# Performance work log

Measured on AMD Instinct MI355X. Metric: run time of the kernel, lower is better.

Reference implementation:

```python
import jax, jax.numpy as jnp
import numpy as np

N = 100000      # nodes
E = 1600000     # edges
D_IN = 16       # input_dim
D_H = 32        # hidden_dim
D_OUT = 1       # output_dim
N_ITERS = 2
D_CAT = D_H + D_IN          # node feature after cat([H, X])
D_EDGE = 2 * D_CAT          # edge MLP input dim


def setup_inputs() -> dict:
    key = jax.random.key(0)
    ks = jax.random.split(key, 10)
    x = jax.random.normal(ks[0], (N, D_IN), jnp.float32)
    edge_index = jax.random.randint(ks[1], (2, E), 0, N, dtype=jnp.int32)
    # inputnet: Linear(D_IN -> D_H) + Tanh
    W_in = jax.random.normal(ks[2], (D_H, D_IN), jnp.float32) / np.sqrt(D_IN)
    b_in = jnp.zeros((D_H,), jnp.float32)
    # convnn (EdgeConv nn): Linear(D_EDGE -> D_H) + Sigmoid
    W_c = jax.random.normal(ks[3], (D_H, D_EDGE), jnp.float32) / np.sqrt(D_EDGE)
    b_c = jnp.zeros((D_H,), jnp.float32)
    # outputnet: Linear(D_H -> D_OUT) + Sigmoid
    W_out = jax.random.normal(ks[4], (D_OUT, D_H), jnp.float32) / np.sqrt(D_H)
    b_out = jnp.zeros((D_OUT,), jnp.float32)
    return {"x": x, "edge_index": edge_index, "W_in": W_in, "b_in": b_in,
            "W_c": W_c, "b_c": b_c, "W_out": W_out, "b_out": b_out}


def reference(x, edge_index, W_in, b_in, W_c, b_c, W_out, b_out):
    src = edge_index[0]  # x_j (source / neighbor)
    dst = edge_index[1]  # x_i (target, aggregation index)

    H = jnp.tanh(x @ W_in.T + b_in)            # [N, D_H]
    feats = jnp.concatenate([H, x], axis=-1)    # [N, D_CAT]

    for _ in range(N_ITERS):
        xi = feats[dst]                          # [E, D_CAT] gather targets
        xj = feats[src]                          # [E, D_CAT] gather sources
        # PyG EdgeConv message: nn(cat([x_i, x_j - x_i]))
        msg = jax.nn.sigmoid(
            jnp.concatenate([xi, xj - xi], axis=-1) @ W_c.T + b_c)  # [E, D_H]
        H = jax.ops.segment_sum(msg, dst, num_segments=N)           # aggr='add'
        feats = jnp.concatenate([H, x], axis=-1)

    sum_H = jnp.mean(H, axis=0)                  # [D_H]
    return jax.nn.sigmoid(sum_H @ W_out.T + b_out)  # [D_OUT]
```

## Files before the change

kernel.cpp:

```cpp
#include <hip/hip_runtime.h>
#include <hip/hip_fp16.h>

#define D_H 32
#define NREP 32
#define SLOTS 48
#define BIN_SHIFT 8
#define MAXNB 512
#define BIN_CAP 5120
#define SB 256
#define PNPB 64
#define SF 52
#define L2E 1.4426950408889634f


__global__ __launch_bounds__(256) void k_ab0(const float* __restrict__ x,
                      const float* __restrict__ W_in, const float* __restrict__ b_in,
                      const float* __restrict__ W_c, const float* __restrict__ b_c,
                      float* __restrict__ A, __half* __restrict__ Bh, int N) {
    __shared__ float f[PNPB][SF];
    int tid = threadIdx.x;
    int n0 = blockIdx.x * PNPB;
    int wv = tid >> 6;
    int h  = (tid >> 5) & 1;
    int j  = tid & 31;
    float wc[96];
    {
        const float4* wr = (const float4*)(W_c + j * 96);
#pragma unroll
        for (int q = 0; q < 24; ++q) {
            float4 v = wr[q];
            wc[4 * q] = v.x; wc[4 * q + 1] = v.y; wc[4 * q + 2] = v.z; wc[4 * q + 3] = v.w;
        }
    }
    float win[16];
    {
        const float4* wr = (const float4*)(W_in + j * 16);
#pragma unroll
        for (int q = 0; q < 4; ++q) {
            float4 v = wr[q];
            win[4 * q] = v.x; win[4 * q + 1] = v.y; win[4 * q + 2] = v.z; win[4 * q + 3] = v.w;
        }
    }
    float bc = b_c[j];
    float bi = b_in[j];
    {
        int row = tid >> 2, c = tid & 3;
        float4 v = {0.f, 0.f, 0.f, 0.f};
        if (n0 + row < N) v = ((const float4*)(x + (size_t)(n0 + row) * 16))[c];
        *(float4*)&f[row][32 + 4 * c] = v;
    }
    __syncthreads();
#pragma unroll 2
    for (int it = 0; it < 8; ++it) {
        int n = wv * 16 + it * 2 + h;
        {
            float4 x0 = *(const float4*)&f[n][32];
            float4 x1 = *(const float4*)&f[n][36];
            float4 x2 = *(const float4*)&f[n][40];
            float4 x3 = *(const float4*)&f[n][44];
            float acc = bi;
            acc += x0.x * win[0] + x0.y * win[1] + x0.z * win[2] + x0.w * win[3];
            acc += x1.x * win[4] + x1.y * win[5] + x1.z * win[6] + x1.w * win[7];
            acc += x2.x * win[8] + x2.y * win[9] + x2.z * win[10] + x2.w * win[11];
            acc += x3.x * win[12] + x3.y * win[13] + x3.z * win[14] + x3.w * win[15];
            f[n][j] = tanhf(acc);
        }
        float p = bc, bb = 0.f;
#pragma unroll
        for (int q = 0; q < 12; ++q) {
            float4 v = *(const float4*)&f[n][4 * q];
            p  += v.x * wc[4 * q]      + v.y * wc[4 * q + 1]
                + v.z * wc[4 * q + 2]  + v.w * wc[4 * q + 3];
            bb += v.x * wc[48 + 4 * q]     + v.y * wc[48 + 4 * q + 1]
                + v.z * wc[48 + 4 * q + 2] + v.w * wc[48 + 4 * q + 3];
        }
        int g = n0 + n;
        if (g < N) {
            A[(size_t)g * D_H + j]  = -L2E * (p - bb);
            Bh[(size_t)g * D_H + j] = __float2half_rn(-L2E * bb);
        }
    }
}

__global__ __launch_bounds__(256) void k_ab1(const float* __restrict__ H,
                      const float* __restrict__ x, const float* __restrict__ W_c,
                      const float* __restrict__ b_c, float* __restrict__ A,
                      __half* __restrict__ Bh, int N) {
    __shared__ float f[PNPB][SF];
    int tid = threadIdx.x;
    int n0 = blockIdx.x * PNPB;
    int wv = tid >> 6;
    int h  = (tid >> 5) & 1;
    int j  = tid & 31;
    float wc[96];
    {
        const float4* wr = (const float4*)(W_c + j * 96);
#pragma unroll
        for (int q = 0; q < 24; ++q) {
            float4 v = wr[q];
            wc[4 * q] = v.x; wc[4 * q + 1] = v.y; wc[4 * q + 2] = v.z; wc[4 * q + 3] = v.w;
        }
    }
    float bc = b_c[j];
#pragma unroll
    for (int k = 0; k < 2; ++k) {
        int i = k * 256 + tid;
        int row = i >> 3, c = i & 7;
        float4 v = {0.f, 0.f, 0.f, 0.f};
        if (n0 + row < N) v = ((const float4*)(H + (size_t)(n0 + row) * D_H))[c];
        *(float4*)&f[row][4 * c] = v;
    }
    {
        int row = tid >> 2, c = tid & 3;
        float4 v = {0.f, 0.f, 0.f, 0.f};
        if (n0 + row < N) v = ((const float4*)(x + (size_t)(n0 + row) * 16))[c];
        *(float4*)&f[row][32 + 4 * c] = v;
    }
    __syncthreads();
#pragma unroll 2
    for (int it = 0; it < 8; ++it) {
        int n = wv * 16 + it * 2 + h;
        float p = bc, bb = 0.f;
#pragma unroll
        for (int q = 0; q < 12; ++q) {
            float4 v = *(const float4*)&f[n][4 * q];
            p  += v.x * wc[4 * q]      + v.y * wc[4 * q + 1]
                + v.z * wc[4 * q + 2]  + v.w * wc[4 * q + 3];
            bb += v.x * wc[48 + 4 * q]     + v.y * wc[48 + 4 * q + 1]
                + v.z * wc[48 + 4 * q + 2] + v.w * wc[48 + 4 * q + 3];
        }
        int g = n0 + n;
        if (g < N) {
            A[(size_t)g * D_H + j]  = -L2E * (p - bb);
            Bh[(size_t)g * D_H + j] = __float2half_rn(-L2E * bb);
        }
    }
}

__global__ __launch_bounds__(256) void k_bin(const int* __restrict__ src,
                                             const int* __restrict__ dst,
                                             int* __restrict__ binCnt,
                                             unsigned int* __restrict__ ebuf, int E) {
    __shared__ int hist[MAXNB];
    int tid = threadIdx.x;
    for (int i = tid; i < MAXNB; i += 256) hist[i] = 0;
    __syncthreads();
    int chunk = (E + SB - 1) / SB;
    int lo = blockIdx.x * chunk;
    int hi = lo + chunk; if (hi > E) hi = E;
    for (int e = lo + tid; e < hi; e += 256) {
        int b = dst[e] >> BIN_SHIFT;
        atomicAdd(&hist[b], 1);
    }
    __syncthreads();
    for (int b = tid; b < MAXNB; b += 256) {
        int c = hist[b];
        int base = c ? atomicAdd(&binCnt[b], c) : 0;
        hist[b] = b * BIN_CAP + base;
    }
    __syncthreads();
    for (int e = lo + tid; e < hi; e += 256) {
        int d = dst[e];
        int s = src[e];
        int b = d >> BIN_SHIFT;
        int pos = atomicAdd(&hist[b], 1);
        if ((unsigned)(pos - b * BIN_CAP) < (unsigned)BIN_CAP)
            ebuf[pos] = ((unsigned)(d & 255) << 24) | (unsigned)s;
    }
}

__global__ __launch_bounds__(256) void k_place(const int* __restrict__ binCnt,
                                               const unsigned int* __restrict__ ebuf,
                                               int* __restrict__ ssrcp,
                                               int* __restrict__ cntG,
                                               float* __restrict__ Srep, int N) {
    __shared__ int cnt[256];
    int tid = threadIdx.x;
    int w = blockIdx.x;
    if (w == 0) {
        float4 z = {0.f, 0.f, 0.f, 0.f};
        ((float4*)Srep)[tid] = z;
    }
    cnt[tid] = 0;
    __syncthreads();
    int n = binCnt[w]; if (n > BIN_CAP) n = BIN_CAP;
    int base = w * BIN_CAP;
    for (int j = tid; j < n; j += 256) {
        unsigned int v = ebuf[base + j];
        int ld = v >> 24;
        int s = v & 0xFFFFFF;
        int slot = atomicAdd(&cnt[ld], 1);
        if (slot < SLOTS)
            ssrcp[(size_t)((w << BIN_SHIFT) + ld) * SLOTS + slot] = s;
    }
    __syncthreads();
    int node = (w << BIN_SHIFT) + tid;
    if (node < N) {
        int c = cnt[tid] < SLOTS ? cnt[tid] : SLOTS;
        cntG[node] = c;
        int cp = (c + 3) & ~3;
        for (int t2 = c; t2 < cp; ++t2)
            ssrcp[(size_t)node * SLOTS + t2] = 0;
    }
}


__global__ __launch_bounds__(256) void k_gather1(const int* __restrict__ cntG,
                          const int* __restrict__ ssrcp,
                          const float* __restrict__ A, const __half* __restrict__ Bh,
                          float* __restrict__ H, int N) {
    int t = blockIdx.x * blockDim.x + threadIdx.x;
    int d = t >> 5;
    if (d >= N) return;
    int l = t & 31;
    int q = l & 7;
    int s = l >> 3;
    int len = cntG[d];
    const int* base = ssrcp + (size_t)d * SLOTS;
    float4 a4 = ((const float4*)(A + (size_t)d * D_H))[q];
    float4 acc = {0.f, 0.f, 0.f, 0.f};
    for (int bj = 0; bj < len; bj += 16) {
        int jj = bj + 4 * s;
        if (jj < len) {
            int4 iv = *(const int4*)(base + jj);
            int rem = len - jj;
#pragma unroll
            for (int k = 0; k < 4; ++k) {
                int idx = ((const int*)&iv)[k];
                float vld = (k < rem) ? 1.f : 0.f;
                uint2 u = *(const uint2*)(Bh + (size_t)idx * D_H + 4 * q);
                __half2 h0 = *reinterpret_cast<const __half2*>(&u.x);
                __half2 h1 = *reinterpret_cast<const __half2*>(&u.y);
                float2 f0 = __half22float2(h0);
                float2 f1 = __half22float2(h1);
                float e0 = exp2f(a4.x + f0.x);
                float e1 = exp2f(a4.y + f0.y);
                float e2 = exp2f(a4.z + f1.x);
                float e3 = exp2f(a4.w + f1.y);
                acc.x = fmaf(vld, __builtin_amdgcn_rcpf(1.f + e0), acc.x);
                acc.y = fmaf(vld, __builtin_amdgcn_rcpf(1.f + e1), acc.y);
                acc.z = fmaf(vld, __builtin_amdgcn_rcpf(1.f + e2), acc.z);
                acc.w = fmaf(vld, __builtin_amdgcn_rcpf(1.f + e3), acc.w);
            }
        }
    }
    acc.x += __shfl_xor(acc.x, 8);  acc.y += __shfl_xor(acc.y, 8);
    acc.z += __shfl_xor(acc.z, 8);  acc.w += __shfl_xor(acc.w, 8);
    acc.x += __shfl_xor(acc.x, 16); acc.y += __shfl_xor(acc.y, 16);
    acc.z += __shfl_xor(acc.z, 16); acc.w += __shfl_xor(acc.w, 16);
    if (s == 0) ((float4*)(H + (size_t)d * D_H))[q] = acc;
}

__global__ __launch_bounds__(256) void k_gather2(const int* __restrict__ cntG,
                          const int* __restrict__ ssrcp,
                          const float* __restrict__ A, const __half* __restrict__ Bh,
                          float* __restrict__ Srep, int N) {
    int l = threadIdx.x & 31;
    int slot = threadIdx.x >> 5;
    int q = l & 7;
    int s = l >> 3;
    int d = blockIdx.x * 8 + slot;
    float4 acc = {0.f, 0.f, 0.f, 0.f};
    if (d < N) {
        int len = cntG[d];
        const int* base = ssrcp + (size_t)d * SLOTS;
        float4 a4 = ((const float4*)(A + (size_t)d * D_H))[q];
        for (int bj = 0; bj < len; bj += 16) {
            int jj = bj + 4 * s;
            if (jj < len) {
                int4 iv = *(const int4*)(base + jj);
                int rem = len - jj;
#pragma unroll
                for (int k = 0; k < 4; ++k) {
                    int idx = ((const int*)&iv)[k];
                    float vld = (k < rem) ? 1.f : 0.f;
                    uint2 u = *(const uint2*)(Bh + (size_t)idx * D_H + 4 * q);
                    __half2 h0 = *reinterpret_cast<const __half2*>(&u.x);
                    __half2 h1 = *reinterpret_cast<const __half2*>(&u.y);
                    float2 f0 = __half22float2(h0);
                    float2 f1 = __half22float2(h1);
                    float e0 = exp2f(a4.x + f0.x);
                    float e1 = exp2f(a4.y + f0.y);
                    float e2 = exp2f(a4.z + f1.x);
                    float e3 = exp2f(a4.w + f1.y);
                    acc.x = fmaf(vld, __builtin_amdgcn_rcpf(1.f + e0), acc.x);
                    acc.y = fmaf(vld, __builtin_amdgcn_rcpf(1.f + e1), acc.y);
                    acc.z = fmaf(vld, __builtin_amdgcn_rcpf(1.f + e2), acc.z);
                    acc.w = fmaf(vld, __builtin_amdgcn_rcpf(1.f + e3), acc.w);
                }
            }
        }
    }
    acc.x += __shfl_xor(acc.x, 8);  acc.y += __shfl_xor(acc.y, 8);
    acc.z += __shfl_xor(acc.z, 8);  acc.w += __shfl_xor(acc.w, 8);
    acc.x += __shfl_xor(acc.x, 16); acc.y += __shfl_xor(acc.y, 16);
    acc.z += __shfl_xor(acc.z, 16); acc.w += __shfl_xor(acc.w, 16);
    __shared__ float red[8][32];
    if (s == 0) {
        red[slot][4 * q + 0] = acc.x;
        red[slot][4 * q + 1] = acc.y;
        red[slot][4 * q + 2] = acc.z;
        red[slot][4 * q + 3] = acc.w;
    }
    __syncthreads();
    if (threadIdx.x < 32) {
        float sm = 0.f;
#pragma unroll
        for (int r = 0; r < 8; ++r) sm += red[r][threadIdx.x];
        unsafeAtomicAdd(&Srep[(blockIdx.x & (NREP - 1)) * D_H + threadIdx.x], sm);
    }
}

__global__ void k_final(const float* __restrict__ Srep, const float* __restrict__ W_out,
                        const float* __restrict__ b_out, float* __restrict__ out,
                        float invN) {
    int j = threadIdx.x;
    float v = 0.f;
    if (j < 32) {
        float s = 0.f;
#pragma unroll
        for (int r = 0; r < NREP; ++r) s += Srep[r * D_H + j];
        v = s * invN * W_out[j];
    }
#pragma unroll
    for (int off = 32; off > 0; off >>= 1) v += __shfl_down(v, off);
    if (j == 0) out[0] = 1.f / (1.f + __expf(-(v + b_out[0])));
}

extern "C" void kernel_launch(void* const* d_in, const int* in_sizes, int n_in,
                              void* d_out, int out_size, void* d_ws, size_t ws_size,
                              hipStream_t stream) {
    const float* x     = (const float*)d_in[0];
    const int*   ei    = (const int*)d_in[1];
    const float* W_in  = (const float*)d_in[2];
    const float* b_in  = (const float*)d_in[3];
    const float* W_c   = (const float*)d_in[4];
    const float* b_c   = (const float*)d_in[5];
    const float* W_out = (const float*)d_in[6];
    const float* b_out = (const float*)d_in[7];

    const int N = in_sizes[0] / 16;
    const int E = in_sizes[1] / 2;
    const int* src = ei;
    const int* dst = ei + E;

    const int NB = (N + 255) >> BIN_SHIFT;

    float* H    = (float*)d_ws;
    float* A    = H + (size_t)N * D_H;
    float* Breg = A + (size_t)N * D_H;
    __half* Bh  = (__half*)Breg;
    float* Srep = Breg + (size_t)N * D_H;
    int*   cntG   = (int*)(Srep + NREP * D_H);
    int*   binCnt = cntG + N;
    int*   ssrcp  = binCnt + MAXNB;
    unsigned int* ebuf = (unsigned int*)H;

    float* out = (float*)d_out;

    const int abBlocks = (N + PNPB - 1) / PNPB;

    hipMemsetAsync(binCnt, 0, MAXNB * sizeof(int), stream);
    k_bin<<<SB, 256, 0, stream>>>(src, dst, binCnt, ebuf, E);
    k_place<<<NB, 256, 0, stream>>>(binCnt, ebuf, ssrcp, cntG, Srep, N);

    k_ab0<<<abBlocks, 256, 0, stream>>>(x, W_in, b_in, W_c, b_c, A, Bh, N);
    k_gather1<<<(int)(((size_t)N * 32 + 255) / 256), 256, 0, stream>>>(cntG, ssrcp, A, Bh, H, N);

    k_ab1<<<abBlocks, 256, 0, stream>>>(H, x, W_c, b_c, A, Bh, N);
    k_gather2<<<(N + 7) / 8, 256, 0, stream>>>(cntG, ssrcp, A, Bh, Srep, N);

    k_final<<<1, 64, 0, stream>>>(Srep, W_out, b_out, out, 1.f / (float)N);
}
```

Baseline: 246.6 us.

## Fuse first gather with second-layer A/B projection and unroll slot loop

The first neighbor-gather kernel and the following per-node projection kernel are merged, so each 32-lane group aggregates one node's messages, stores the sum in shared memory, and immediately computes that node's A and B values for the next layer. This removes the H round trip through global memory and one kernel launch. Because the second gather still reads A and B while the fused kernel writes new ones, separate A2/Bh2 buffers are added. The data-dependent slot loop is replaced by three fixed guarded chunks covering the 48-slot cap. In exchange, every small 8-node block reloads the 96 W_c weights per thread, which adds register pressure and redundant weight loads.

```diff
diff --git a/kernel.cpp b/kernel.cpp
--- a/kernel.cpp
+++ b/kernel.cpp
@@ -12,6 +12,34 @@
 #define SF 52
 #define L2E 1.4426950408889634f
 
+__device__ __forceinline__ void gacc4(float4& acc, const float4 a4,
+                                      const int* __restrict__ base, int jb, int len,
+                                      int q, const __half* __restrict__ Bh) {
+    int4 iv = *(const int4*)(base + jb);
+#pragma unroll
+    for (int k = 0; k < 4; ++k) {
+        int idx = ((const int*)&iv)[k];
+        float vld = (jb + k < len) ? 1.f : 0.f;
+        uint2 u = *(const uint2*)(Bh + (size_t)idx * D_H + 4 * q);
+        __half2 h0 = *reinterpret_cast<const __half2*>(&u.x);
+        __half2 h1 = *reinterpret_cast<const __half2*>(&u.y);
+        float2 f0 = __half22float2(h0);
+        float2 f1 = __half22float2(h1);
+        acc.x = fmaf(vld, __builtin_amdgcn_rcpf(1.f + exp2f(a4.x + f0.x)), acc.x);
+        acc.y = fmaf(vld, __builtin_amdgcn_rcpf(1.f + exp2f(a4.y + f0.y)), acc.y);
+        acc.z = fmaf(vld, __builtin_amdgcn_rcpf(1.f + exp2f(a4.z + f1.x)), acc.z);
+        acc.w = fmaf(vld, __builtin_amdgcn_rcpf(1.f + exp2f(a4.w + f1.y)), acc.w);
+    }
+}
+
+__device__ __forceinline__ void gaccAll(float4& acc, const float4 a4,
+                                        const int* __restrict__ base, int len,
+                                        int s, int q, const __half* __restrict__ Bh) {
+    int j0 = 4 * s, j1 = 16 + 4 * s, j2 = 32 + 4 * s;
+    if (j0 < len) gacc4(acc, a4, base, j0, len, q, Bh);
+    if (j1 < len) gacc4(acc, a4, base, j1, len, q, Bh);
+    if (j2 < len) gacc4(acc, a4, base, j2, len, q, Bh);
+}
 
 __global__ __launch_bounds__(256) void k_ab0(const float* __restrict__ x,
                       const float* __restrict__ W_in, const float* __restrict__ b_in,
@@ -82,58 +110,62 @@
     }
 }
 
-__global__ __launch_bounds__(256) void k_ab1(const float* __restrict__ H,
-                      const float* __restrict__ x, const float* __restrict__ W_c,
-                      const float* __restrict__ b_c, float* __restrict__ A,
-                      __half* __restrict__ Bh, int N) {
-    __shared__ float f[PNPB][SF];
+__global__ __launch_bounds__(256) void k_g1ab1(const int* __restrict__ cntG,
+                      const int* __restrict__ ssrcp, const float* __restrict__ A,
+                      const __half* __restrict__ Bh, const float* __restrict__ x,
+                      const float* __restrict__ W_c, const float* __restrict__ b_c,
+                      float* __restrict__ A2, __half* __restrict__ Bh2, int N) {
+    __shared__ float f[8][SF];
     int tid = threadIdx.x;
-    int n0 = blockIdx.x * PNPB;
-    int wv = tid >> 6;
-    int h  = (tid >> 5) & 1;
-    int j  = tid & 31;
+    int n0 = blockIdx.x * 8;
+    int grp = tid >> 5;
+    int l = tid & 31;
+    int q = l & 7;
+    int s = l >> 3;
+    int j = l;
     float wc[96];
     {
         const float4* wr = (const float4*)(W_c + j * 96);
 #pragma unroll
-        for (int q = 0; q < 24; ++q) {
-            float4 v = wr[q];
-            wc[4 * q] = v.x; wc[4 * q + 1] = v.y; wc[4 * q + 2] = v.z; wc[4 * q + 3] = v.w;
+        for (int t = 0; t < 24; ++t) {
+            float4 v = wr[t];
+            wc[4 * t] = v.x; wc[4 * t + 1] = v.y; wc[4 * t + 2] = v.z; wc[4 * t + 3] = v.w;
         }
     }
     float bc = b_c[j];
-#pragma unroll
-    for (int k = 0; k < 2; ++k) {
-        int i = k * 256 + tid;
-        int row = i >> 3, c = i & 7;
-        float4 v = {0.f, 0.f, 0.f, 0.f};
-        if (n0 + row < N) v = ((const float4*)(H + (size_t)(n0 + row) * D_H))[c];
-        *(float4*)&f[row][4 * c] = v;
-    }
-    {
+    if (tid < 32) {
         int row = tid >> 2, c = tid & 3;
         float4 v = {0.f, 0.f, 0.f, 0.f};
         if (n0 + row < N) v = ((const float4*)(x + (size_t)(n0 + row) * 16))[c];
         *(float4*)&f[row][32 + 4 * c] = v;
     }
-    __syncthreads();
-#pragma unroll 2
-    for (int it = 0; it < 8; ++it) {
-        int n = wv * 16 + it * 2 + h;
-        float p = bc, bb = 0.f;
-#pragma unroll
-        for (int q = 0; q < 12; ++q) {
-            float4 v = *(const float4*)&f[n][4 * q];
-            p  += v.x * wc[4 * q]      + v.y * wc[4 * q + 1]
-                + v.z * wc[4 * q + 2]  + v.w * wc[4 * q + 3];
-            bb += v.x * wc[48 + 4 * q]     + v.y * wc[48 + 4 * q + 1]
-                + v.z * wc[48 + 4 * q + 2] + v.w * wc[48 + 4 * q + 3];
-        }
-        int g = n0 + n;
-        if (g < N) {
-            A[(size_t)g * D_H + j]  = -L2E * (p - bb);
-            Bh[(size_t)g * D_H + j] = __float2half_rn(-L2E * bb);
-        }
+    int d = n0 + grp;
+    float4 acc = {0.f, 0.f, 0.f, 0.f};
+    if (d < N) {
+        int len = cntG[d];
+        const int* base = ssrcp + (size_t)d * SLOTS;
+        float4 a4 = ((const float4*)(A + (size_t)d * D_H))[q];
+        gaccAll(acc, a4, base, len, s, q, Bh);
+    }
+    acc.x += __shfl_xor(acc.x, 8);  acc.y += __shfl_xor(acc.y, 8);
+    acc.z += __shfl_xor(acc.z, 8);  acc.w += __shfl_xor(acc.w, 8);
+    acc.x += __shfl_xor(acc.x, 16); acc.y += __shfl_xor(acc.y, 16);
+    acc.z += __shfl_xor(acc.z, 16); acc.w += __shfl_xor(acc.w, 16);
+    if (s == 0) *(float4*)&f[grp][4 * q] = acc;
+    __syncthreads();
+    float p = bc, bb = 0.f;
+#pragma unroll
+    for (int t = 0; t < 12; ++t) {
+        float4 v = *(const float4*)&f[grp][4 * t];
+        p  += v.x * wc[4 * t]      + v.y * wc[4 * t + 1]
+            + v.z * wc[4 * t + 2]  + v.w * wc[4 * t + 3];
+        bb += v.x * wc[48 + 4 * t]     + v.y * wc[48 + 4 * t + 1]
+            + v.z * wc[48 + 4 * t + 2] + v.w * wc[48 + 4 * t + 3];
+    }
+    int g = n0 + grp;
+    if (g < N) {
+        A2[(size_t)g * D_H + j]  = -L2E * (p - bb);
+        Bh2[(size_t)g * D_H + j] = __float2half_rn(-L2E * bb);
     }
 }
 
@@ -202,53 +234,6 @@
         for (int t2 = c; t2 < cp; ++t2)
             ssrcp[(size_t)node * SLOTS + t2] = 0;
     }
-}
-
-
-__global__ __launch_bounds__(256) void k_gather1(const int* __restrict__ cntG,
-                          const int* __restrict__ ssrcp,
-                          const float* __restrict__ A, const __half* __restrict__ Bh,
-                          float* __restrict__ H, int N) {
-    int t = blockIdx.x * blockDim.x + threadIdx.x;
-    int d = t >> 5;
-    if (d >= N) return;
-    int l = t & 31;
-    int q = l & 7;
-    int s = l >> 3;
-    int len = cntG[d];
-    const int* base = ssrcp + (size_t)d * SLOTS;
-    float4 a4 = ((const float4*)(A + (size_t)d * D_H))[q];
-    float4 acc = {0.f, 0.f, 0.f, 0.f};
-    for (int bj = 0; bj < len; bj += 16) {
-        int jj = bj + 4 * s;
-        if (jj < len) {
-            int4 iv = *(const int4*)(base + jj);
-            int rem = len - jj;
-#pragma unroll
-            for (int k = 0; k < 4; ++k) {
-                int idx = ((const int*)&iv)[k];
-                float vld = (k < rem) ? 1.f : 0.f;
-                uint2 u = *(const uint2*)(Bh + (size_t)idx * D_H + 4 * q);
-                __half2 h0 = *reinterpret_cast<const __half2*>(&u.x);
-                __half2 h1 = *reinterpret_cast<const __half2*>(&u.y);
-                float2 f0 = __half22float2(h0);
-                float2 f1 = __half22float2(h1);
-                float e0 = exp2f(a4.x + f0.x);
-                float e1 = exp2f(a4.y + f0.y);
-                float e2 = exp2f(a4.z + f1.x);
-                float e3 = exp2f(a4.w + f1.y);
-                acc.x = fmaf(vld, __builtin_amdgcn_rcpf(1.f + e0), acc.x);
-                acc.y = fmaf(vld, __builtin_amdgcn_rcpf(1.f + e1), acc.y);
-                acc.z = fmaf(vld, __builtin_amdgcn_rcpf(1.f + e2), acc.z);
-                acc.w = fmaf(vld, __builtin_amdgcn_rcpf(1.f + e3), acc.w);
-            }
-        }
-    }
-    acc.x += __shfl_xor(acc.x, 8);  acc.y += __shfl_xor(acc.y, 8);
-    acc.z += __shfl_xor(acc.z, 8);  acc.w += __shfl_xor(acc.w, 8);
-    acc.x += __shfl_xor(acc.x, 16); acc.y += __shfl_xor(acc.y, 16);
-    acc.z += __shfl_xor(acc.z, 16); acc.w += __shfl_xor(acc.w, 16);
-    if (s == 0) ((float4*)(H + (size_t)d * D_H))[q] = acc;
 }
 
 __global__ __launch_bounds__(256) void k_gather2(const int* __restrict__ cntG,
@@ -265,31 +250,7 @@
         int len = cntG[d];
         const int* base = ssrcp + (size_t)d * SLOTS;
         float4 a4 = ((const float4*)(A + (size_t)d * D_H))[q];
-        for (int bj = 0; bj < len; bj += 16) {
-            int jj = bj + 4 * s;
-            if (jj < len) {
-                int4 iv = *(const int4*)(base + jj);
-                int rem = len - jj;
-#pragma unroll
-                for (int k = 0; k < 4; ++k) {
-                    int idx = ((const int*)&iv)[k];
-                    float vld = (k < rem) ? 1.f : 0.f;
-                    uint2 u = *(const uint2*)(Bh + (size_t)idx * D_H + 4 * q);
-                    __half2 h0 = *reinterpret_cast<const __half2*>(&u.x);
-                    __half2 h1 = *reinterpret_cast<const __half2*>(&u.y);
-                    float2 f0 = __half22float2(h0);
-                    float2 f1 = __half22float2(h1);
-                    float e0 = exp2f(a4.x + f0.x);
-                    float e1 = exp2f(a4.y + f0.y);
-                    float e2 = exp2f(a4.z + f1.x);
-                    float e3 = exp2f(a4.w + f1.y);
-                    acc.x = fmaf(vld, __builtin_amdgcn_rcpf(1.f + e0), acc.x);
-                    acc.y = fmaf(vld, __builtin_amdgcn_rcpf(1.f + e1), acc.y);
-                    acc.z = fmaf(vld, __builtin_amdgcn_rcpf(1.f + e2), acc.z);
-                    acc.w = fmaf(vld, __builtin_amdgcn_rcpf(1.f + e3), acc.w);
-                }
-            }
-        }
+        gaccAll(acc, a4, base, len, s, q, Bh);
     }
     acc.x += __shfl_xor(acc.x, 8);  acc.y += __shfl_xor(acc.y, 8);
     acc.z += __shfl_xor(acc.z, 8);  acc.w += __shfl_xor(acc.w, 8);
@@ -346,29 +307,30 @@
 
     const int NB = (N + 255) >> BIN_SHIFT;
 
-    float* H    = (float*)d_ws;
-    float* A    = H + (size_t)N * D_H;
-    float* Breg = A + (size_t)N * D_H;
-    __half* Bh  = (__half*)Breg;
-    float* Srep = Breg + (size_t)N * D_H;
+    float* A2   = (float*)d_ws;
+    float* A    = A2 + (size_t)N * D_H;
+    __half* Bh  = (__half*)(A + (size_t)N * D_H);
+    float* Srep = (float*)(Bh + (size_t)N * D_H);
     int*   cntG   = (int*)(Srep + NREP * D_H);
     int*   binCnt = cntG + N;
     int*   ssrcp  = binCnt + MAXNB;
-    unsigned int* ebuf = (unsigned int*)H;
+    __half* Bh2 = (__half*)(ssrcp + (size_t)N * SLOTS);
+    unsigned int* ebuf = (unsigned int*)A2;
 
     float* out = (float*)d_out;
 
     const int abBlocks = (N + PNPB - 1) / PNPB;
+    const int gBlocks  = (N + 7) / 8;
 
     hipMemsetAsync(binCnt, 0, MAXNB * sizeof(int), stream);
     k_bin<<<SB, 256, 0, stream>>>(src, dst, binCnt, ebuf, E);
     k_place<<<NB, 256, 0, stream>>>(binCnt, ebuf, ssrcp, cntG, Srep, N);
 
     k_ab0<<<abBlocks, 256, 0, stream>>>(x, W_in, b_in, W_c, b_c, A, Bh, N);
-    k_gather1<<<(int)(((size_t)N * 32 + 255) / 256), 256, 0, stream>>>(cntG, ssrcp, A, Bh, H, N);
-
-    k_ab1<<<abBlocks, 256, 0, stream>>>(H, x, W_c, b_c, A, Bh, N);
-    k_gather2<<<(N + 7) / 8, 256, 0, stream>>>(cntG, ssrcp, A, Bh, Srep, N);
+
+    k_g1ab1<<<gBlocks, 256, 0, stream>>>(cntG, ssrcp, A, Bh, x, W_c, b_c, A2, Bh2, N);
+
+    k_gather2<<<gBlocks, 256, 0, stream>>>(cntG, ssrcp, A2, Bh2, Srep, N);
 
     k_final<<<1, 64, 0, stream>>>(Srep, W_out, b_out, out, 1.f / (float)N);
 }
```

Result: slower. 356.3 us (+44.5%).
